# Performance work log

Hardware: AMD Instinct MI355X
Metric: run time of the kernel (lower is better)

The kernel has to match this reference:

```python
import jax, jax.numpy as jnp
import numpy as np

# Each of the 16 soft logic gates in tableOperator is a polynomial
#   gate_t(A,B) = c0 + cA*A + cB*B + cAB*A*B
# _COEFF[t] = [c0, cA, cB, cAB], matching the torch tableOperator rows 0..15.
_COEFF = np.array([
    [0,  0,  0,  0],   # 0: 0
    [0,  0,  0,  1],   # 1: A*B
    [0,  1,  0, -1],   # 2: A - A*B
    [0,  1,  0,  0],   # 3: A
    [0,  0,  1, -1],   # 4: B - A*B
    [0,  0,  1,  0],   # 5: B
    [0,  1,  1, -2],   # 6: A + B - 2AB
    [0,  1,  1, -1],   # 7: A + B - AB
    [1, -1, -1,  1],   # 8: 1 - (A + B - AB)
    [1, -1, -1,  2],   # 9: 1 - (A + B - 2AB)
    [1,  0, -1,  0],   # 10: 1 - B
    [1,  0, -1,  1],   # 11: 1 - B + AB
    [1, -1,  0,  0],   # 12: 1 - A
    [1, -1,  0,  1],   # 13: 1 - A + AB
    [1,  0,  0, -1],   # 14: 1 - AB
    [1,  0,  0,  0],   # 15: 1
], dtype=np.float32)

PREV_SIZE, SIZE, BATCH = 2048, 2048, 8192

def setup_inputs() -> dict:
    key = jax.random.key(0)
    k1, k2, k3, k4 = jax.random.split(key, 4)
    return {
        "prev_layer_output": jax.random.uniform(k1, (PREV_SIZE, BATCH), dtype=jnp.float32),
        "input_A_weights": jax.random.normal(k2, (SIZE, PREV_SIZE), dtype=jnp.float32) * 0.05,
        "input_B_weights": jax.random.normal(k3, (SIZE, PREV_SIZE), dtype=jnp.float32) * 0.05,
        "table_weights": jax.random.normal(k4, (16, SIZE), dtype=jnp.float32) * 0.05,
    }

def reference(prev_layer_output, input_A_weights, input_B_weights, table_weights):
    # Training (grad-enabled) path of LogicLayer.forward; GradFactor(x, 1) is identity.
    pA = jax.nn.softmax(input_A_weights, axis=1)   # [size, prev_size]
    pB = jax.nn.softmax(input_B_weights, axis=1)   # [size, prev_size]
    pT = jax.nn.softmax(table_weights, axis=0)     # [16, size]
    A = pA @ prev_layer_output                     # [size, batch]
    B = pB @ prev_layer_output                     # [size, batch]
    # Fuse sum_t pT[t] * gate_t(A,B): contract gate coefficients with table probs.
    c = jnp.einsum('tc,ts->cs', jnp.asarray(_COEFF), pT)  # [4, size]
    out = (c[0][:, None]
           + c[1][:, None] * A
           + c[2][:, None] * B
           + c[3][:, None] * (A * B))               # [size, batch]
    return out
```

## Files before the change

kernel.cpp:

```cpp
#include <hip/hip_runtime.h>
#include <hip/hip_bf16.h>

#define M_DIM 2048
#define K_DIM 2048
#define N_DIM 8192

#define BM 128
#define BN 256
#define BK 128
#define NT (K_DIM / BK)

typedef __attribute__((ext_vector_type(4))) int i32x4;

static __device__ __forceinline__ void stage1k(const unsigned char* g, void* l) {
    __builtin_amdgcn_global_load_lds(
        (const __attribute__((address_space(1))) void*)g,
        (__attribute__((address_space(3))) void*)l, 16, 0, 0);
}

__global__ __launch_bounds__(256) void prep_kernel(
    const float* __restrict__ prev, const float* __restrict__ Wa,
    const float* __restrict__ Wb, const float* __restrict__ TW,
    unsigned char* __restrict__ Pa, unsigned char* __restrict__ Pb,
    unsigned char* __restrict__ Pt,
    float* __restrict__ SA, float* __restrict__ SB, float4* __restrict__ C4)
{
    __shared__ unsigned char tile[64][80];
    __shared__ float redm[4], reds[4];
    const int bx = blockIdx.x;
    const int t = threadIdx.x;

    if (bx < 4096) {
        const int n0 = (bx & 127) * 64;
        const int k0 = (bx >> 7) * 64;
        const int kb = (t >> 4) * 4;
        const int nb = (t & 15) * 4;
        unsigned int pk0 = 0, pk1 = 0, pk2 = 0, pk3 = 0;
#pragma unroll
        for (int j = 0; j < 4; ++j) {
            float4 v = *(const float4*)(prev + (size_t)(k0 + kb + j) * N_DIM + n0 + nb);
            pk0 |= (unsigned int)(unsigned char)(int)(127.f * v.x + 0.5f) << (8 * j);
            pk1 |= (unsigned int)(unsigned char)(int)(127.f * v.y + 0.5f) << (8 * j);
            pk2 |= (unsigned int)(unsigned char)(int)(127.f * v.z + 0.5f) << (8 * j);
            pk3 |= (unsigned int)(unsigned char)(int)(127.f * v.w + 0.5f) << (8 * j);
        }
        *(unsigned int*)&tile[nb + 0][kb] = pk0;
        *(unsigned int*)&tile[nb + 1][kb] = pk1;
        *(unsigned int*)&tile[nb + 2][kb] = pk2;
        *(unsigned int*)&tile[nb + 3][kb] = pk3;
        __syncthreads();
        const int n = t >> 2;
        const int k16 = (t & 3) * 16;
        int4 v = *(const int4*)&tile[n][k16];
        *(int4*)(Pt + (size_t)(n0 + n) * K_DIM + k0 + k16) = v;
        return;
    }
    if (bx < 8192) {
        const int r = bx - 4096;
        const int row = r & 2047;
        const int isB = r >> 11;
        const float* W = isB ? Wb : Wa;
        unsigned char* P = isB ? Pb : Pa;
        float* S = isB ? SB : SA;
        const float* w = W + (size_t)row * K_DIM + t * 8;
        float4 v0 = *(const float4*)(w);
        float4 v1 = *(const float4*)(w + 4);
        float x[8] = {v0.x, v0.y, v0.z, v0.w, v1.x, v1.y, v1.z, v1.w};

        float m = x[0];
#pragma unroll
        for (int i = 1; i < 8; ++i) m = fmaxf(m, x[i]);
#pragma unroll
        for (int off = 32; off >= 1; off >>= 1) m = fmaxf(m, __shfl_xor(m, off));
        const int wid = t >> 6;
        if ((t & 63) == 0) redm[wid] = m;
        __syncthreads();
        m = fmaxf(fmaxf(redm[0], redm[1]), fmaxf(redm[2], redm[3]));

        float s = 0.f;
#pragma unroll
        for (int i = 0; i < 8; ++i) { x[i] = __expf(x[i] - m); s += x[i]; }
#pragma unroll
        for (int off = 32; off >= 1; off >>= 1) s += __shfl_xor(s, off);
        if ((t & 63) == 0) reds[wid] = s;
        __syncthreads();
        s = reds[0] + reds[1] + reds[2] + reds[3];

        union { unsigned char u[8]; int2 v; } pk;
#pragma unroll
        for (int i = 0; i < 8; ++i)
            pk.u[i] = (unsigned char)(int)(127.f * x[i] + 0.5f);
        *(int2*)(P + (size_t)row * K_DIM + t * 8) = pk.v;
        if (t == 0) S[row] = 1.f / (16129.f * s);
        return;
    }
    const int s = (bx - 8192) * 256 + t;
    if (s >= M_DIM) return;
    float x[16];
    float m = -1e30f;
#pragma unroll
    for (int tt = 0; tt < 16; ++tt) { x[tt] = TW[tt * M_DIM + s]; m = fmaxf(m, x[tt]); }
    float sum = 0.f;
#pragma unroll
    for (int tt = 0; tt < 16; ++tt) { x[tt] = __expf(x[tt] - m); sum += x[tt]; }
    const float inv = 1.0f / sum;
    const float c0a[16] = {0,0,0,0,0,0,0,0, 1,1,1,1,1,1,1,1};
    const float cAa[16] = {0,0,1,1,0,0,1,1, -1,-1,0,0,-1,-1,0,0};
    const float cBa[16] = {0,0,0,0,1,1,1,1, -1,-1,-1,-1,0,0,0,0};
    const float cXa[16] = {0,1,-1,0,-1,0,-2,-1, 1,2,0,1,0,1,-1,0};
    float c0 = 0.f, cA = 0.f, cB = 0.f, cX = 0.f;
#pragma unroll
    for (int tt = 0; tt < 16; ++tt) {
        const float p = x[tt] * inv;
        c0 += p * c0a[tt]; cA += p * cAa[tt]; cB += p * cBa[tt]; cX += p * cXa[tt];
    }
    C4[s] = make_float4(c0, cA, cB, cX);
}


#define MFMA8(ACC, FA, FP, MI0)                                                \
    _Pragma("unroll") for (int mi = (MI0); mi < (MI0) + 2; ++mi)               \
    _Pragma("unroll") for (int ni = 0; ni < 4; ++ni)                           \
        ACC[mi][ni] = __builtin_amdgcn_mfma_i32_16x16x64_i8(                   \
            FA[mi], FP[ni], ACC[mi][ni], 0, 0, 0);

#define STAGE_A(T) do { const int b_ = (T) & 1; const size_t o_ = (size_t)(T) * BK; \
    stage1k(gPa + o_,  &sPa[b_][0][wid * 16][0]);                              \
    stage1k(gPt0 + o_, &sPt[b_][0][wid * 16][0]); } while (0)
#define STAGE_B(T) do { const int b_ = (T) & 1; const size_t o_ = (size_t)(T) * BK; \
    stage1k(gPt1 + o_, &sPt[b_][0][128 + wid * 16][0]);                        \
    stage1k(gPb + o_,  &sPb[b_][0][wid * 16][0]); } while (0)
#define STAGE_C(T) do { const int b_ = (T) & 1; const size_t o_ = (size_t)(T) * BK + 64; \
    stage1k(gPa + o_,  &sPa[b_][1][wid * 16][0]);                              \
    stage1k(gPt0 + o_, &sPt[b_][1][wid * 16][0]); } while (0)
#define STAGE_D(T) do { const int b_ = (T) & 1; const size_t o_ = (size_t)(T) * BK + 64; \
    stage1k(gPt1 + o_, &sPt[b_][1][128 + wid * 16][0]);                        \
    stage1k(gPb + o_,  &sPb[b_][1][wid * 16][0]); } while (0)

#define RD_SET(FA, FB, FP, BA, BB, BP)                                         \
    _Pragma("unroll") for (int i = 0; i < 4; ++i)                              \
        FA[i] = *(const i32x4*)((BA) + roA + i * 1024);                        \
    _Pragma("unroll") for (int i = 0; i < 4; ++i)                              \
        FP[i] = *(const i32x4*)((BP) + roP + i * 1024);                        \
    _Pragma("unroll") for (int i = 0; i < 4; ++i)                              \
        FB[i] = *(const i32x4*)((BB) + roA + i * 1024);

__global__ __launch_bounds__(512, 2) void logic_gemm_kernel(
    const unsigned char* __restrict__ Pa,
    const unsigned char* __restrict__ Pb,
    const unsigned char* __restrict__ Pt,
    const float4* __restrict__ C4,
    const float* __restrict__ SA,
    const float* __restrict__ SB,
    float* __restrict__ out)
{
    __shared__ unsigned char sPa[2][2][128][64];
    __shared__ unsigned char sPb[2][2][128][64];
    __shared__ unsigned char sPt[2][2][256][64];

    const int m0 = blockIdx.y * BM;
    const int n0 = blockIdx.x * BN;
    const int t = threadIdx.x;
    const int wid = t >> 6, lane = t & 63;
    const int wr = wid >> 2, wc = wid & 3;
    const int lq = lane >> 4, lr = lane & 15;

    const int srow = lane >> 2;
    const int scol = (((lane & 3) ^ ((lane >> 3) & 3)) << 4);
    const unsigned char* gPa  = Pa + (size_t)(m0 + wid * 16 + srow) * K_DIM + scol;
    const unsigned char* gPb  = Pb + (size_t)(m0 + wid * 16 + srow) * K_DIM + scol;
    const unsigned char* gPt0 = Pt + (size_t)(n0 + wid * 16 + srow) * K_DIM + scol;
    const unsigned char* gPt1 = gPt0 + (size_t)128 * K_DIM;

    const int cswz = (lq ^ ((lr >> 1) & 3)) << 4;
    const int roA = (wr * 64 + lr) * 64 + cswz;
    const int roP = (wc * 64 + lr) * 64 + cswz;

    i32x4 accA[4][4] = {};
    i32x4 accB[4][4] = {};
    i32x4 fa0[4], fb0[4], fp0[4], fa1[4], fb1[4], fp1[4];

    STAGE_A(0); STAGE_B(0); STAGE_C(0); STAGE_D(0);
    STAGE_A(1); STAGE_B(1);
    asm volatile("s_waitcnt vmcnt(4)" ::: "memory");
    __builtin_amdgcn_s_barrier();
    RD_SET(fa0, fb0, fp0,
           (const char*)&sPa[0][0][0][0],
           (const char*)&sPb[0][0][0][0],
           (const char*)&sPt[0][0][0][0]);

    for (int kt = 0; kt < NT; ++kt) {
        const int buf = kt & 1;
        const char* bA1 = (const char*)&sPa[buf][1][0][0];
        const char* bB1 = (const char*)&sPb[buf][1][0][0];
        const char* bP1 = (const char*)&sPt[buf][1][0][0];
        const char* nA0 = (const char*)&sPa[buf ^ 1][0][0][0];
        const char* nB0 = (const char*)&sPb[buf ^ 1][0][0][0];
        const char* nP0 = (const char*)&sPt[buf ^ 1][0][0][0];

        __builtin_amdgcn_s_setprio(1);
        MFMA8(accA, fa0, fp0, 0);
        MFMA8(accA, fa0, fp0, 2);
        __builtin_amdgcn_s_setprio(0);
        RD_SET(fa1, fb1, fp1, bA1, bB1, bP1);
        if (kt + 1 < NT) { STAGE_C(kt + 1); STAGE_D(kt + 1); }
        if (kt < NT - 1) asm volatile("s_waitcnt vmcnt(4)" ::: "memory");
        else             asm volatile("s_waitcnt vmcnt(0)" ::: "memory");
        __builtin_amdgcn_s_setprio(1);
        MFMA8(accB, fb0, fp0, 0);
        MFMA8(accB, fb0, fp0, 2);
        __builtin_amdgcn_s_setprio(0);
        __builtin_amdgcn_s_barrier();

        __builtin_amdgcn_s_setprio(1);
        MFMA8(accA, fa1, fp1, 0);
        MFMA8(accA, fa1, fp1, 2);
        __builtin_amdgcn_s_setprio(0);
        if (kt + 1 < NT) RD_SET(fa0, fb0, fp0, nA0, nB0, nP0);
        if (kt + 2 < NT) { STAGE_A(kt + 2); STAGE_B(kt + 2); }
        if (kt < NT - 2) asm volatile("s_waitcnt vmcnt(4)" ::: "memory");
        else             asm volatile("s_waitcnt vmcnt(0)" ::: "memory");
        __builtin_amdgcn_s_setprio(1);
        MFMA8(accB, fb1, fp1, 0);
        MFMA8(accB, fb1, fp1, 2);
        __builtin_amdgcn_s_setprio(0);
        __builtin_amdgcn_s_barrier();
    }

#pragma unroll
    for (int mi = 0; mi < 4; ++mi) {
#pragma unroll
        for (int i = 0; i < 4; ++i) {
            const int row = m0 + wr * 64 + mi * 16 + lq * 4 + i;
            const float4 c = C4[row];
            const float sa = SA[row];
            const float sb = SB[row];
#pragma unroll
            for (int ni = 0; ni < 4; ++ni) {
                const int col = n0 + wc * 64 + ni * 16 + lr;
                const float Av = (float)accA[mi][ni][i] * sa;
                const float Bv = (float)accB[mi][ni][i] * sb;
                out[(size_t)row * N_DIM + col] = c.x + c.y * Av + c.z * Bv + c.w * Av * Bv;
            }
        }
    }
}

extern "C" void kernel_launch(void* const* d_in, const int* in_sizes, int n_in,
                              void* d_out, int out_size, void* d_ws, size_t ws_size,
                              hipStream_t stream) {
    const float* prev = (const float*)d_in[0];
    const float* Wa   = (const float*)d_in[1];
    const float* Wb   = (const float*)d_in[2];
    const float* TW   = (const float*)d_in[3];
    float* out = (float*)d_out;

    char* ws = (char*)d_ws;
    unsigned char* Pa = (unsigned char*)(ws);
    unsigned char* Pb = (unsigned char*)(ws + (size_t)(4u << 20));
    unsigned char* Pt = (unsigned char*)(ws + (size_t)(8u << 20));
    float4* C4 = (float4*)(ws + (size_t)(24u << 20));
    float*  SA = (float*)(ws + (size_t)(24u << 20) + (32u << 10));
    float*  SB = (float*)(ws + (size_t)(24u << 20) + (64u << 10));

    prep_kernel<<<dim3(8200), 256, 0, stream>>>(prev, Wa, Wb, TW,
                                                Pa, Pb, Pt, SA, SB, C4);
    logic_gemm_kernel<<<dim3(N_DIM / BN, M_DIM / BM), 512, 0, stream>>>(Pa, Pb, Pt, C4, SA, SB, out);
}
```

Measured before the change: 83.25 us.

## Shrink GEMM tile to 128x128x64 with 4 waves and triple-buffered LDS

Changes the int8 dual-GEMM kernel from 512-thread 128x256 tiles with a hand-interleaved double-buffer and K=128 split schedule to 256-thread 128x128 tiles with K=64 steps and a three-stage LDS ring. Each iteration issues the prefetch two stages ahead, loads fragments, runs all MFMAs, then waits and barriers once. The simpler schedule uses less LDS per block and launches twice as many blocks, in exchange for more barriers per K, loss of LDS-read/MFMA interleaving, and re-reading A/B operands for each N tile.

```diff
diff --git a/kernel.cpp b/kernel.cpp
--- a/kernel.cpp
+++ b/kernel.cpp
@@ -6,8 +6,8 @@
 #define N_DIM 8192
 
 #define BM 128
-#define BN 256
-#define BK 128
+#define BN 128
+#define BK 64
 #define NT (K_DIM / BK)
 
 typedef __attribute__((ext_vector_type(4))) int i32x4;
@@ -124,28 +124,16 @@
         ACC[mi][ni] = __builtin_amdgcn_mfma_i32_16x16x64_i8(                   \
             FA[mi], FP[ni], ACC[mi][ni], 0, 0, 0);
 
-#define STAGE_A(T) do { const int b_ = (T) & 1; const size_t o_ = (size_t)(T) * BK; \
-    stage1k(gPa + o_,  &sPa[b_][0][wid * 16][0]);                              \
-    stage1k(gPt0 + o_, &sPt[b_][0][wid * 16][0]); } while (0)
-#define STAGE_B(T) do { const int b_ = (T) & 1; const size_t o_ = (size_t)(T) * BK; \
-    stage1k(gPt1 + o_, &sPt[b_][0][128 + wid * 16][0]);                        \
-    stage1k(gPb + o_,  &sPb[b_][0][wid * 16][0]); } while (0)
-#define STAGE_C(T) do { const int b_ = (T) & 1; const size_t o_ = (size_t)(T) * BK + 64; \
-    stage1k(gPa + o_,  &sPa[b_][1][wid * 16][0]);                              \
-    stage1k(gPt0 + o_, &sPt[b_][1][wid * 16][0]); } while (0)
-#define STAGE_D(T) do { const int b_ = (T) & 1; const size_t o_ = (size_t)(T) * BK + 64; \
-    stage1k(gPt1 + o_, &sPt[b_][1][128 + wid * 16][0]);                        \
-    stage1k(gPb + o_,  &sPb[b_][1][wid * 16][0]); } while (0)
-
-#define RD_SET(FA, FB, FP, BA, BB, BP)                                         \
-    _Pragma("unroll") for (int i = 0; i < 4; ++i)                              \
-        FA[i] = *(const i32x4*)((BA) + roA + i * 1024);                        \
-    _Pragma("unroll") for (int i = 0; i < 4; ++i)                              \
-        FP[i] = *(const i32x4*)((BP) + roP + i * 1024);                        \
-    _Pragma("unroll") for (int i = 0; i < 4; ++i)                              \
-        FB[i] = *(const i32x4*)((BB) + roA + i * 1024);
-
-__global__ __launch_bounds__(512, 2) void logic_gemm_kernel(
+#define STAGE(T) do { const int b_ = (T) % 3;                                  \
+    const size_t o_ = (size_t)(T) * BK;                                        \
+    stage1k(gPa + o_,               &sPa[b_][wid * 16][0]);                    \
+    stage1k(gPa + o_ + 64 * K_DIM,  &sPa[b_][64 + wid * 16][0]);               \
+    stage1k(gPb + o_,               &sPb[b_][wid * 16][0]);                    \
+    stage1k(gPb + o_ + 64 * K_DIM,  &sPb[b_][64 + wid * 16][0]);               \
+    stage1k(gPt + o_,               &sPt[b_][wid * 16][0]);                    \
+    stage1k(gPt + o_ + 64 * K_DIM,  &sPt[b_][64 + wid * 16][0]); } while (0)
+
+__global__ __launch_bounds__(256, 2) void logic_gemm_kernel(
     const unsigned char* __restrict__ Pa,
     const unsigned char* __restrict__ Pb,
     const unsigned char* __restrict__ Pt,
@@ -154,23 +142,22 @@
     const float* __restrict__ SB,
     float* __restrict__ out)
 {
-    __shared__ unsigned char sPa[2][2][128][64];
-    __shared__ unsigned char sPb[2][2][128][64];
-    __shared__ unsigned char sPt[2][2][256][64];
+    __shared__ unsigned char sPa[3][128][64];
+    __shared__ unsigned char sPb[3][128][64];
+    __shared__ unsigned char sPt[3][128][64];
 
     const int m0 = blockIdx.y * BM;
     const int n0 = blockIdx.x * BN;
     const int t = threadIdx.x;
     const int wid = t >> 6, lane = t & 63;
-    const int wr = wid >> 2, wc = wid & 3;
+    const int wr = wid >> 1, wc = wid & 1;
     const int lq = lane >> 4, lr = lane & 15;
 
     const int srow = lane >> 2;
     const int scol = (((lane & 3) ^ ((lane >> 3) & 3)) << 4);
-    const unsigned char* gPa  = Pa + (size_t)(m0 + wid * 16 + srow) * K_DIM + scol;
-    const unsigned char* gPb  = Pb + (size_t)(m0 + wid * 16 + srow) * K_DIM + scol;
-    const unsigned char* gPt0 = Pt + (size_t)(n0 + wid * 16 + srow) * K_DIM + scol;
-    const unsigned char* gPt1 = gPt0 + (size_t)128 * K_DIM;
+    const unsigned char* gPa = Pa + (size_t)(m0 + wid * 16 + srow) * K_DIM + scol;
+    const unsigned char* gPb = Pb + (size_t)(m0 + wid * 16 + srow) * K_DIM + scol;
+    const unsigned char* gPt = Pt + (size_t)(n0 + wid * 16 + srow) * K_DIM + scol;
 
     const int cswz = (lq ^ ((lr >> 1) & 3)) << 4;
     const int roA = (wr * 64 + lr) * 64 + cswz;
@@ -178,52 +165,37 @@
 
     i32x4 accA[4][4] = {};
     i32x4 accB[4][4] = {};
-    i32x4 fa0[4], fb0[4], fp0[4], fa1[4], fb1[4], fp1[4];
-
-    STAGE_A(0); STAGE_B(0); STAGE_C(0); STAGE_D(0);
-    STAGE_A(1); STAGE_B(1);
-    asm volatile("s_waitcnt vmcnt(4)" ::: "memory");
+    i32x4 fa[4], fb[4], fp[4];
+
+    STAGE(0);
+    STAGE(1);
+    asm volatile("s_waitcnt vmcnt(6)" ::: "memory");
     __builtin_amdgcn_s_barrier();
-    RD_SET(fa0, fb0, fp0,
-           (const char*)&sPa[0][0][0][0],
-           (const char*)&sPb[0][0][0][0],
-           (const char*)&sPt[0][0][0][0]);
 
     for (int kt = 0; kt < NT; ++kt) {
-        const int buf = kt & 1;
-        const char* bA1 = (const char*)&sPa[buf][1][0][0];
-        const char* bB1 = (const char*)&sPb[buf][1][0][0];
-        const char* bP1 = (const char*)&sPt[buf][1][0][0];
-        const char* nA0 = (const char*)&sPa[buf ^ 1][0][0][0];
-        const char* nB0 = (const char*)&sPb[buf ^ 1][0][0][0];
-        const char* nP0 = (const char*)&sPt[buf ^ 1][0][0][0];
+        const int bcur = kt % 3;
+        const char* bA = (const char*)&sPa[bcur][0][0];
+        const char* bB = (const char*)&sPb[bcur][0][0];
+        const char* bP = (const char*)&sPt[bcur][0][0];
+
+        if (kt + 2 < NT) STAGE(kt + 2);
+
+#pragma unroll
+        for (int i = 0; i < 4; ++i) fa[i] = *(const i32x4*)(bA + roA + i * 1024);
+#pragma unroll
+        for (int i = 0; i < 4; ++i) fp[i] = *(const i32x4*)(bP + roP + i * 1024);
+#pragma unroll
+        for (int i = 0; i < 4; ++i) fb[i] = *(const i32x4*)(bB + roA + i * 1024);
 
         __builtin_amdgcn_s_setprio(1);
-        MFMA8(accA, fa0, fp0, 0);
-        MFMA8(accA, fa0, fp0, 2);
+        MFMA8(accA, fa, fp, 0);
+        MFMA8(accA, fa, fp, 2);
+        MFMA8(accB, fb, fp, 0);
+        MFMA8(accB, fb, fp, 2);
         __builtin_amdgcn_s_setprio(0);
-        RD_SET(fa1, fb1, fp1, bA1, bB1, bP1);
-        if (kt + 1 < NT) { STAGE_C(kt + 1); STAGE_D(kt + 1); }
-        if (kt < NT - 1) asm volatile("s_waitcnt vmcnt(4)" ::: "memory");
+
+        if (kt < NT - 2) asm volatile("s_waitcnt vmcnt(6)" ::: "memory");
         else             asm volatile("s_waitcnt vmcnt(0)" ::: "memory");
-        __builtin_amdgcn_s_setprio(1);
-        MFMA8(accB, fb0, fp0, 0);
-        MFMA8(accB, fb0, fp0, 2);
-        __builtin_amdgcn_s_setprio(0);
-        __builtin_amdgcn_s_barrier();
-
-        __builtin_amdgcn_s_setprio(1);
-        MFMA8(accA, fa1, fp1, 0);
-        MFMA8(accA, fa1, fp1, 2);
-        __builtin_amdgcn_s_setprio(0);
-        if (kt + 1 < NT) RD_SET(fa0, fb0, fp0, nA0, nB0, nP0);
-        if (kt + 2 < NT) { STAGE_A(kt + 2); STAGE_B(kt + 2); }
-        if (kt < NT - 2) asm volatile("s_waitcnt vmcnt(4)" ::: "memory");
-        else             asm volatile("s_waitcnt vmcnt(0)" ::: "memory");
-        __builtin_amdgcn_s_setprio(1);
-        MFMA8(accB, fb1, fp1, 0);
-        MFMA8(accB, fb1, fp1, 2);
-        __builtin_amdgcn_s_setprio(0);
         __builtin_amdgcn_s_barrier();
     }
 
@@ -265,5 +237,5 @@
 
     prep_kernel<<<dim3(8200), 256, 0, stream>>>(prev, Wa, Wb, TW,
                                                 Pa, Pb, Pt, SA, SB, C4);
-    logic_gemm_kernel<<<dim3(N_DIM / BN, M_DIM / BM), 512, 0, stream>>>(Pa, Pb, Pt, C4, SA, SB, out);
-}
+    logic_gemm_kernel<<<dim3(N_DIM / BN, M_DIM / BM), 256, 0, stream>>>(Pa, Pb, Pt, C4, SA, SB, out);
+}
```

Result: slower. 96.35 us (+15.7%).
